# Optimization experiments

Hardware: AMD Instinct MI355X
Metric: run time of the kernel (lower is better)

The kernel has to match this reference:

```python
import math
import jax, jax.numpy as jnp
import numpy as np

# ---- static configuration (matches init_kwargs) ----
BATCH, F_IN, F_OUT = 8, 64, 128
B_IN, B_OUT = 32, 16
NL = B_OUT                    # spherical degrees l = 0..NL-1
MDIM = 2 * NL - 1             # dense order axis, m in [-(NL-1), NL-1]
N_BETA_G, N_ALPHA_G = 4, 8
MAX_BETA = math.pi / 8
N_GRID = N_BETA_G * N_ALPHA_G
SCALING = 1.0 / math.sqrt(N_GRID * F_IN * B_OUT ** 4.0 / B_IN ** 2.0)

_LF = np.concatenate([[0.0], np.cumsum(np.log(np.arange(1, 200, dtype=np.float64)))])  # log n!

def _wigner_d(l, betas):
    """Wigner small-d d^l_{m1,m2}(beta) -> [len(betas), 2l+1, 2l+1]."""
    m1 = np.arange(-l, l + 1).reshape(-1, 1, 1)
    m2 = np.arange(-l, l + 1).reshape(1, -1, 1)
    k = np.arange(0, 2 * l + 1).reshape(1, 1, -1)
    a1, a3, a4 = l + m2 - k, m1 - m2 + k, l - m1 - k
    valid = (a1 >= 0) & (a3 >= 0) & (a4 >= 0)
    logc = (0.5 * (_LF[l + m1] + _LF[l - m1] + _LF[l + m2] + _LF[l - m2])
            - _LF[np.clip(a1, 0, None)] - _LF[k]
            - _LF[np.clip(a3, 0, None)] - _LF[np.clip(a4, 0, None)])
    coef = np.where(valid, ((-1.0) ** (m1 - m2 + k)) * np.exp(logc), 0.0)
    c = np.cos(betas / 2.0)[:, None, None, None]
    s = np.sin(betas / 2.0)[:, None, None, None]
    ce = np.clip(2 * l + m2 - m1 - 2 * k, 0, None)
    se = np.clip(m1 - m2 + 2 * k, 0, None)
    return (coef[None] * (c ** ce) * (s ** se)).sum(-1)

# SOFT beta sampling grids
_betas_in = np.pi * (2 * np.arange(2 * B_IN) + 0.5) / (4 * B_IN)
_betas_out = np.pi * (2 * np.arange(2 * B_OUT) + 0.5) / (4 * B_OUT)

# Driscoll-Healy quadrature weights on the input beta grid (alpha measure 2pi/(2b) folded in)
_kk = np.arange(B_IN)
_w = ((2.0 * np.pi / (2 * B_IN)) * (2.0 / B_IN) * np.sin(_betas_in)
      * (np.sin(_betas_in[:, None] * (2 * _kk + 1)) / (2 * _kk + 1)).sum(1))

# kernel grid: s2_near_identity_grid(max_beta=pi/8, n_alpha=8, n_beta=4), beta-major order
_gb = MAX_BETA * np.arange(1, N_BETA_G + 1) / N_BETA_G
_ga = 2 * np.pi * np.arange(N_ALPHA_G) / N_ALPHA_G
GRID_BETA, GRID_ALPHA = [a.ravel() for a in np.meshgrid(_gb, _ga, indexing='ij')]

# W_ANA[beta_j, l, m]  = w_j * d^l_{m,0}(beta_j)            (S2 analysis)
# D_SYN[l, beta_k, m, n] = (2l+1) * d^l_{m,n}(beta_k)       (SO3 synthesis)
# FK[g, l, m]          = d^l_{m,0}(beta_g) * e^{i m alpha_g} (kernel real-FT, s2_rft)
W_ANA = np.zeros((2 * B_IN, NL, MDIM), np.float32)
D_SYN = np.zeros((NL, 2 * B_OUT, MDIM, MDIM), np.float32)
FK = np.zeros((N_GRID, NL, MDIM), np.complex64)
for l in range(NL):
    sl = slice(NL - 1 - l, NL + l)  # dense slots for m = -l..l
    W_ANA[:, l, sl] = (_w[:, None] * _wigner_d(l, _betas_in)[:, :, l]).astype(np.float32)
    D_SYN[l, :, sl, sl] = ((2 * l + 1) * _wigner_d(l, _betas_out)).astype(np.float32)
    m = np.arange(-l, l + 1)
    FK[:, l, sl] = (_wigner_d(l, GRID_BETA)[:, :, l]
                    * np.exp(1j * m[None, :] * GRID_ALPHA[:, None])).astype(np.complex64)
W_ANA, D_SYN, FK = jnp.asarray(W_ANA), jnp.asarray(D_SYN), jnp.asarray(FK)

_M_VALS = np.arange(-(NL - 1), NL)
_BINS_IN = _M_VALS % (2 * B_IN)  # fft bins of the alpha-frequencies m=-15..15


def setup_inputs() -> dict:
    key = jax.random.key(0)
    k1, k2 = jax.random.split(key)
    x = jax.random.normal(k1, (BATCH, F_IN, 2 * B_IN, 2 * B_IN), jnp.float32)
    kernel = jax.random.uniform(k2, (F_IN, F_OUT, N_GRID), jnp.float32, -1.0, 1.0)
    bias = jnp.zeros((1, F_OUT, 1, 1, 1), jnp.float32)
    return {"x": x, "kernel": kernel, "bias": bias}


def _s2_conv(x, kernel, bias):
    # ---- S2 FFT of the input: [B,Fin,2b_in(beta),2b_in(alpha)] -> spectrum [l,m,B,Fin] ----
    xf = jnp.fft.fft(x, axis=-1)              # e^{-i m alpha}
    xm = xf[..., _BINS_IN]                    # [B, Fin, 2b_in, MDIM]
    xhat = jnp.einsum('jlm,bfjm->lmbf', W_ANA, xm)            # [NL, MDIM, B, Fin] complex

    # ---- kernel spherical-harmonic expansion (s2_rft) ----
    kh = jnp.einsum('iog,glm->lmio', (kernel * SCALING).astype(jnp.complex64), FK)

    # ---- per-degree block matmul (s2_mm): z^l_{mn} = sum_i xhat^l_m[i] conj(kh^l_n[i]) ----
    z = jnp.einsum('lmbi,lnio->lmnbo', xhat, jnp.conj(kh))    # [NL, MDIM, MDIM, B, Fout]

    # ---- inverse SO(3) FFT: sum over degrees with (2l+1) d^l_{mn}(beta), then ifft2 over (alpha,gamma) ----
    fmn = jnp.einsum('lkmn,lmnbo->bokmn', D_SYN, z)           # [B, Fout, 2b_out, MDIM, MDIM]
    g = jnp.zeros((BATCH, F_OUT, 2 * B_OUT, 2 * B_OUT, 2 * B_OUT), fmn.dtype)
    g = g.at[..., :MDIM, :MDIM].set(fmn)
    g = jnp.roll(g, shift=(-(NL - 1), -(NL - 1)), axis=(-2, -1))  # m=0 at fft bin 0
    out = jnp.fft.ifft2(g, axes=(-2, -1)).real * float((2 * B_OUT) ** 2)  # e^{+i m alpha}
    return out.astype(jnp.float32) + bias


def reference(x, kernel, bias):
    return _s2_conv(x, kernel, bias)
```

## Files before the change

kernel.cpp:

```cpp
#include <hip/hip_runtime.h>
#include <stdint.h>
#include <math.h>


#define PI_D 3.14159265358979323846
#define SCALING_F 0.002762135864009951f

#define OFF_WANA 0
#define OFF_FKR  31744
#define OFF_FKI  47616
#define OFF_D3   63488
#define OFF_XHAT 317440
#define OFF_WT   317440
#define OFF_KHC  825344
#define OFF_Z2   3053568
#define OFF_T    11180032

typedef unsigned short u16t;
typedef __attribute__((ext_vector_type(8))) short s8v;
typedef __attribute__((ext_vector_type(8))) _Float16 h8v;
typedef __attribute__((ext_vector_type(4))) float f4v;

union frg { uint4 u; uint32_t w[4]; s8v s; h8v h; };

__device__ inline double ipow_d(double x, int e){
  double r = 1.0;
  while (e > 0){ if (e & 1) r *= x; x *= x; e >>= 1; }
  return r;
}

__device__ double wig_d(int l, int m1, int m2, double beta, const double* LF){
  double c = cos(0.5*beta), s = sin(0.5*beta);
  double sum = 0.0;
  for (int k = 0; k <= 2*l; ++k){
    int a1 = l + m2 - k, a3 = m1 - m2 + k, a4 = l - m1 - k;
    if (a1 < 0 || a3 < 0 || a4 < 0) continue;
    double logc = 0.5*(LF[l+m1]+LF[l-m1]+LF[l+m2]+LF[l-m2]) - LF[a1] - LF[k] - LF[a3] - LF[a4];
    double t = exp(logc) * ipow_d(c, a1 + a4) * ipow_d(s, a3 + k);
    sum += (a3 & 1) ? -t : t;
  }
  return sum;
}

__device__ inline uint32_t f2bf(float f){
  uint32_t u = __float_as_uint(f);
  return (u + 0x7fffu + ((u >> 16) & 1u)) >> 16;
}
__device__ inline float bf2f(uint32_t h){ return __uint_as_float((h & 0xffffu) << 16); }
__device__ inline float bf2f_lo(uint32_t h){ return __uint_as_float(h << 16); }
__device__ inline float bf2f_hi(uint32_t h){ return __uint_as_float(h & 0xffff0000u); }
__device__ inline uint32_t pack2(float a, float b){ return f2bf(a) | (f2bf(b) << 16); }

#define LF_INIT \
  __shared__ double LF[40]; \
  if (threadIdx.x == 0){ LF[0] = 0.0; double acc_ = 0.0; for (int n_ = 1; n_ < 40; ++n_){ acc_ += log((double)n_); LF[n_] = acc_; } } \
  __syncthreads();

__global__ void k_zero(float* __restrict__ ws){
  int id = blockIdx.x*256 + threadIdx.x;
  *reinterpret_cast<float4*>(ws + OFF_D3 + (size_t)id*4) = make_float4(0.f,0.f,0.f,0.f);
}

__global__ void k_consts(float* __restrict__ ws){
  LF_INIT
  int bid = blockIdx.x, tid = threadIdx.x;
  if (bid < 124){
    __shared__ double wj2[2];
    int id0 = bid*256;
    int jbase = id0/496;
    if (tid < 2){
      int j = jbase + tid;
      double wv_ = 0.0;
      if (j < 64){
        double beta = PI_D*(2*j + 0.5)/128.0;
        double wsum = 0.0;
        for (int kk = 0; kk < 32; ++kk) wsum += sin(beta*(2*kk+1))/(double)(2*kk+1);
        wv_ = (2.0*PI_D/64.0)*(2.0/32.0)*sin(beta)*wsum;
      }
      wj2[tid] = wv_;
    }
    __syncthreads();
    int id = id0 + tid;
    int m = id % 31, l = (id / 31) & 15, j = id / 496;
    int mp = m - 15, amp = mp < 0 ? -mp : mp;
    float val = 0.f;
    if (amp <= l){
      double beta = PI_D*(2*j + 0.5)/128.0;
      val = (float)(wj2[j - jbase] * wig_d(l, mp, 0, beta, LF));
    }
    ws[OFF_WANA + (l*31 + m)*64 + j] = val;
  } else if (bid < 186){
    int id = (bid - 124)*256 + tid;
    if (id >= 15872) return;
    int n = id % 31, l = (id / 31) & 15, g = id / 496;
    int np = n - 15, anp = np < 0 ? -np : np;
    float vr = 0.f, vi = 0.f;
    if (anp <= l){
      double beta = PI_D*((double)((g >> 3) + 1))/32.0;
      double alpha = (PI_D/4.0)*(double)(g & 7);
      double d = wig_d(l, np, 0, beta, LF);
      vr = (float)(d*cos(np*alpha));
      vi = (float)(d*sin(np*alpha));
    }
    ws[OFF_FKR + id] = vr;
    ws[OFF_FKI + id] = vi;
  } else if (bid < 698){
    int bb = bid - 186;
    int k = bb >> 4, l = bb & 15;
    int n21 = 2*l + 1, items = (l+1)*n21;
    double beta = PI_D*(2*k + 0.5)/64.0;
    float fl = (float)(2*l + 1);
    u16t* d3b = reinterpret_cast<u16t*>(ws + OFF_D3);
    for (int item = tid; item < items; item += 256){
      int im = item / n21, in = item - (item/n21)*n21;
      int mn = im*31 + in - l + 15;
      float v = fl * (float)wig_d(l, im, in - l, beta, LF);
      uint32_t hb = f2bf(v);
      uint32_t lb = f2bf(v - bf2f(hb));
      d3b[(mn*32 + k)*32 + l]      = (u16t)hb;
      d3b[(mn*32 + k)*32 + 16 + l] = (u16t)lb;
    }
  } else {
    u16t* wt = reinterpret_cast<u16t*>(ws + OFF_WT);
    for (int idx = tid; idx < 4096; idx += 256){
      int kidx = idx & 31, cc = (idx >> 5) & 15, h = (idx >> 9) & 1;
      int p = (idx >> 10) & 1, nt = (idx >> 11) & 1;
      int q = kidx & 1, nloc = kidx >> 1, n = h*16 + nloc, cg = nt*16 + cc;
      float val = 0.f;
      if (n <= 30){
        double th = 2.0*PI_D*(double)(((17 + n)*cg) & 31)/32.0;
        float wr = (float)cos(th), wi = (float)sin(th);
        val = p ? (q ? wr : wi) : (q ? -wi : wr);
      }
      union { _Float16 hh[2]; u16t us[2]; } cv;
      cv.hh[0] = (_Float16)val; cv.hh[1] = (_Float16)0.f;
      wt[idx] = cv.us[0];
    }
  }
}

__global__ void k_xhat(const float* __restrict__ x, float* __restrict__ ws){
  __shared__ float xl[4096];
  __shared__ float c64[64], s64[64];
  __shared__ float xmr[1024], xmi[1024];
  int tid = threadIdx.x;
  int b = blockIdx.x >> 6, i = blockIdx.x & 63;
  const float* xp = x + (b*64 + i)*4096;
  for (int idx = tid; idx < 4096; idx += 256) xl[idx] = xp[idx];
  if (tid < 64){ double a = 2.0*PI_D*tid/64.0; c64[tid] = (float)cos(a); s64[tid] = (float)sin(a); }
  __syncthreads();
  for (int item = tid; item < 1024; item += 256){
    int j = item >> 4, mi = item & 15;
    float re = 0.f, im = 0.f;
    const float* xr = xl + j*64;
    for (int a = 0; a < 64; ++a){
      int p = (mi*a) & 63;
      re += xr[a]*c64[p];
      im -= xr[a]*s64[p];
    }
    xmr[item] = re; xmi[item] = im;
  }
  __syncthreads();
  {
    int l = tid >> 4, mi = tid & 15;
    if (mi <= l){
      float rr = 0.f, ri = 0.f;
      const float* wrow = ws + OFF_WANA + (l*31 + 15 + mi)*64;
      for (int j = 0; j < 64; ++j){
        float w = wrow[j];
        rr += w * xmr[j*16 + mi];
        ri += w * xmi[j*16 + mi];
      }
      int dst = OFF_XHAT + ((l*31 + 15 + mi)*8 + b)*128 + i*2;
      ws[dst] = rr; ws[dst+1] = ri;
    }
  }
}

__global__ void k_khc(const float* __restrict__ kern, float* __restrict__ ws){
  __shared__ float kl2[32*66];
  __shared__ float fr[992], fi[992];
  int tid = threadIdx.x;
  int o = blockIdx.x >> 4, l = blockIdx.x & 15;
  for (int idx = tid; idx < 2048; idx += 256){
    int i = idx >> 5, g = idx & 31;
    kl2[g*66 + i] = kern[(i*128 + o)*32 + g];
  }
  for (int idx = tid; idx < 992; idx += 256){
    int g = idx / 31, n = idx - (idx/31)*31;
    fr[idx] = ws[OFF_FKR + g*496 + l*31 + n];
    fi[idx] = ws[OFF_FKI + g*496 + l*31 + n];
  }
  __syncthreads();
  uint32_t* khb = reinterpret_cast<uint32_t*>(ws + OFF_KHC);
  int c1 = (l*(l+1)) >> 1;
  int ntask = (l+1)*32;
  for (int t = tid; t < ntask; t += 256){
    int np = t >> 5, ip = t & 31, i0 = 2*ip;
    float ar0=0.f, ai0=0.f, ar1=0.f, ai1=0.f;
    for (int g = 0; g < 32; ++g){
      float2 kv = *reinterpret_cast<const float2*>(kl2 + g*66 + i0);
      float fv = fr[g*31 + 15 + np], gv = fi[g*31 + 15 + np];
      ar0 += kv.x*fv; ai0 -= kv.x*gv;
      ar1 += kv.y*fv; ai1 -= kv.y*gv;
    }
    size_t base = (size_t)((c1 + np)*128 + o)*64 + i0;
    khb[base]     = pack2(SCALING_F*ar0, SCALING_F*ai0);
    khb[base + 1] = pack2(SCALING_F*ar1, SCALING_F*ai1);
  }
}

__device__ inline int zswz(int o){ return (o ^ (o >> 3)) & 7; }

__global__ __launch_bounds__(512) void k_zmt(float* __restrict__ ws){
  __shared__ uint32_t lb[2][9216];
  __shared__ uint32_t zout[16384];
  int tid = threadIdx.x, lane = tid & 63, wv = tid >> 6;
  int c = lane & 15, g = lane >> 4;
  int bid = blockIdx.x;
  int b = bid / 62, t = bid - b*62;
  int nd = t >> 1, h = t & 1;
  int ndp = nd - 15, a = ndp < 0 ? -ndp : ndp;
  int neg = ndp < 0;
  int l_lo = a > 8*h ? a : 8*h;
  int l_hi = 8*h + 7;

  for (int i = tid; i < 16384; i += 512) zout[i] = 0u;

  const uint32_t* khb = reinterpret_cast<const uint32_t*>(ws + OFF_KHC);

  if (l_lo <= l_hi){
    size_t rowb = (size_t)((l_lo*(l_lo+1))/2 + a)*128;
    #pragma unroll
    for (int t4 = 0; t4 < 4; ++t4){
      int idx4 = t4*512 + tid;
      int o = idx4 >> 4, i4 = idx4 & 15;
      uint4 v = *reinterpret_cast<const uint4*>(khb + (rowb + o)*64 + i4*4);
      *reinterpret_cast<uint4*>(lb[0] + ((o*64 + i4*4) ^ ((o & 7) << 2))) = v;
    }
    int m = tid >> 5, i0 = (tid & 31)*2;
    uint32_t a0 = 0u, a1 = 0u;
    if (m <= l_lo){
      float4 xv = *reinterpret_cast<const float4*>(ws + OFF_XHAT + (((l_lo*31 + 15 + m)*8 + b)*128 + i0*2));
      a0 = pack2(xv.x, xv.y); a1 = pack2(xv.z, xv.w);
    }
    int ai_ = (m*64 + i0) ^ ((m & 7) << 2);
    lb[0][8192 + ai_] = a0; lb[0][8192 + ai_ + 1] = a1;
  }
  __syncthreads();

  int cur = 0;
  for (int l = l_lo; l <= l_hi; ++l){
    uint4 pB[4]; float4 pA = make_float4(0.f,0.f,0.f,0.f);
    int pm = tid >> 5, pi0 = (tid & 31)*2;
    bool pf = (l < l_hi);
    if (pf){
      int lx = l + 1;
      size_t rowb = (size_t)((lx*(lx+1))/2 + a)*128;
      #pragma unroll
      for (int t4 = 0; t4 < 4; ++t4){
        int idx4 = t4*512 + tid;
        int o = idx4 >> 4, i4 = idx4 & 15;
        pB[t4] = *reinterpret_cast<const uint4*>(khb + (rowb + o)*64 + i4*4);
      }
      if (pm <= lx)
        pA = *reinterpret_cast<const float4*>(ws + OFF_XHAT + (((lx*31 + 15 + pm)*8 + b)*128 + pi0*2));
    }
    uint32_t* B = lb[cur];
    uint32_t* A = lb[cur] + 8192;
    frg af[4];
    #pragma unroll
    for (int tt = 0; tt < 4; ++tt)
      af[tt].u = *reinterpret_cast<const uint4*>(A + ((c*64 + tt*16 + g*4) ^ ((c & 7) << 2)));
    int oc = wv*16 + c;
    f4v ar = {0.f,0.f,0.f,0.f}, ai = {0.f,0.f,0.f,0.f};
    #pragma unroll
    for (int tt = 0; tt < 4; ++tt){
      frg bw;
      bw.u = *reinterpret_cast<const uint4*>(B + ((oc*64 + tt*16 + g*4) ^ ((oc & 7) << 2)));
      frg br_, bi_;
      #pragma unroll
      for (int j = 0; j < 4; ++j){
        uint32_t w = bw.w[j];
        uint32_t sw = (w >> 16) | (w << 16);
        if (!neg){ br_.w[j] = w ^ 0x80000000u; bi_.w[j] = sw; }
        else if (a & 1){ br_.w[j] = w ^ 0x80008000u; bi_.w[j] = sw ^ 0x80000000u; }
        else { br_.w[j] = w; bi_.w[j] = sw ^ 0x00008000u; }
      }
      ar = __builtin_amdgcn_mfma_f32_16x16x32_bf16(af[tt].s, br_.s, ar, 0, 0, 0);
      ai = __builtin_amdgcn_mfma_f32_16x16x32_bf16(af[tt].s, bi_.s, ai, 0, 0, 0);
    }
    int lq = l - 8*h;
    #pragma unroll
    for (int rr = 0; rr < 4; ++rr){
      int m = g*4 + rr;
      zout[(m*128 + oc)*8 + (lq ^ zswz(oc))] = pack2(ar[rr], ai[rr]);
    }
    if (pf){
      uint32_t* D = lb[cur ^ 1];
      #pragma unroll
      for (int t4 = 0; t4 < 4; ++t4){
        int idx4 = t4*512 + tid;
        int o = idx4 >> 4, i4 = idx4 & 15;
        *reinterpret_cast<uint4*>(D + ((o*64 + i4*4) ^ ((o & 7) << 2))) = pB[t4];
      }
      int ai_ = (pm*64 + pi0) ^ ((pm & 7) << 2);
      uint32_t a0 = 0u, a1 = 0u;
      if (pm <= l + 1){ a0 = pack2(pA.x, pA.y); a1 = pack2(pA.z, pA.w); }
      D[8192 + ai_] = a0; D[8192 + ai_ + 1] = a1;
    }
    __syncthreads();
    cur ^= 1;
  }

  u16t* zr = reinterpret_cast<u16t*>(ws + OFF_Z2);
  u16t* zi = zr + 8126464;
  for (int idx = tid; idx < 2048; idx += 512){
    int m = idx >> 7, o = idx & 127;
    uint32_t v[8];
    #pragma unroll
    for (int lq = 0; lq < 8; ++lq) v[lq] = zout[(m*128 + o)*8 + (lq ^ zswz(o))];
    uint4 reQ = make_uint4((v[0]&0xffffu)|(v[1]<<16), (v[2]&0xffffu)|(v[3]<<16),
                           (v[4]&0xffffu)|(v[5]<<16), (v[6]&0xffffu)|(v[7]<<16));
    uint4 imQ = make_uint4((v[0]>>16)|(v[1]&0xffff0000u), (v[2]>>16)|(v[3]&0xffff0000u),
                           (v[4]>>16)|(v[5]&0xffff0000u), (v[6]>>16)|(v[7]&0xffff0000u));
    size_t base = (size_t)(m*31 + nd)*16384 + (size_t)(b*128 + o)*16 + h*8;
    *reinterpret_cast<uint4*>(zr + base) = reQ;
    *reinterpret_cast<uint4*>(zi + base) = imQ;
  }
}

__global__ __launch_bounds__(512) void k_fmt(float* __restrict__ ws){
  __shared__ uint32_t fmb[16384];
  int tid = threadIdx.x;
  int lane = tid & 63, wv = tid >> 6;
  int c = lane & 15, g = lane >> 4;
  int bt = blockIdx.x >> 4, m = blockIdx.x & 15;
  const u16t* z2r = reinterpret_cast<const u16t*>(ws + OFF_Z2);
  const u16t* z2i = z2r + 8126464;
  const u16t* d3b = reinterpret_cast<const u16t*>(ws + OFF_D3);
  const u16t* wtb = reinterpret_cast<const u16t*>(ws + OFF_WT);
  fmb[31*512 + (tid ^ 16)] = 0u;

  frg wf[2][2][2];
  #pragma unroll
  for (int nt = 0; nt < 2; ++nt)
    #pragma unroll
    for (int p = 0; p < 2; ++p)
      #pragma unroll
      for (int h = 0; h < 2; ++h)
        wf[nt][p][h].u = *reinterpret_cast<const uint4*>(wtb + ((((nt*2+p)*2+h)*16 + c)*32 + g*8));

  {
    int l0 = (g & 1)*8;
    int hl16 = (g >> 1)*16;
    size_t bo16 = (size_t)(bt*16 + c)*16;
    #pragma unroll
    for (int t = 0; t < 4; ++t){
      int nd = wv*4 + t;
      if (nd > 30) break;
      int mn = m*31 + nd;
      frg ar, ai;
      ar.u = *reinterpret_cast<const uint4*>(z2r + (size_t)mn*16384 + bo16 + l0);
      ai.u = *reinterpret_cast<const uint4*>(z2i + (size_t)mn*16384 + bo16 + l0);
      int key = ((nd >> 2) & 1) << 4;
      #pragma unroll
      for (int kh = 0; kh < 2; ++kh){
        frg bf;
        bf.u = *reinterpret_cast<const uint4*>(d3b + ((size_t)mn*32 + kh*16 + c)*32 + hl16 + l0);
        f4v z4 = {0.f, 0.f, 0.f, 0.f};
        f4v cre = __builtin_amdgcn_mfma_f32_16x16x32_bf16(ar.s, bf.s, z4, 0, 0, 0);
        f4v cim = __builtin_amdgcn_mfma_f32_16x16x32_bf16(ai.s, bf.s, z4, 0, 0, 0);
        #pragma unroll
        for (int rr = 0; rr < 4; ++rr){
          int bok = (g*4 + rr)*32 + kh*16 + c;
          union { _Float16 hh[2]; uint32_t u; } pk;
          pk.hh[0] = (_Float16)cre[rr];
          pk.hh[1] = (_Float16)cim[rr];
          fmb[nd*512 + (bok ^ key)] = pk.u;
        }
      }
    }
  }
  __syncthreads();
  uint32_t* tglob = reinterpret_cast<uint32_t*>(ws) + OFF_T;
  #pragma unroll
  for (int q = 0; q < 4; ++q){
    int mt = wv*4 + q;
    int arow = mt*16 + c;
    frg A0, A1;
    #pragma unroll
    for (int j = 0; j < 4; ++j){
      int nd0 = g*4 + j, nd1 = nd0 + 16;
      A0.w[j] = fmb[nd0*512 + (arow ^ (((nd0 >> 2) & 1) << 4))];
      A1.w[j] = fmb[nd1*512 + (arow ^ (((nd1 >> 2) & 1) << 4))];
    }
    #pragma unroll
    for (int nt = 0; nt < 2; ++nt){
      f4v z4 = {0.f, 0.f, 0.f, 0.f};
      f4v tre = __builtin_amdgcn_mfma_f32_16x16x32_f16(A0.h, wf[nt][0][0].h, z4, 0, 0, 0);
      tre     = __builtin_amdgcn_mfma_f32_16x16x32_f16(A1.h, wf[nt][0][1].h, tre, 0, 0, 0);
      f4v tim = __builtin_amdgcn_mfma_f32_16x16x32_f16(A0.h, wf[nt][1][0].h, z4, 0, 0, 0);
      tim     = __builtin_amdgcn_mfma_f32_16x16x32_f16(A1.h, wf[nt][1][1].h, tim, 0, 0, 0);
      #pragma unroll
      for (int rr = 0; rr < 4; ++rr){
        int bokl = mt*16 + g*4 + rr;
        int bokg = (bt*16 + (bokl >> 5))*32 + (bokl & 31);
        tglob[(size_t)(bokg*16 + m)*32 + nt*16 + c] = pack2(tre[rr], tim[rr]);
      }
    }
  }
}

__global__ void k_out(const float* __restrict__ bias, float* __restrict__ out,
                      const float* __restrict__ ws){
  __shared__ uint32_t tl[2048];
  __shared__ float2 tw2[32];
  int tid = threadIdx.x;
  int b4 = blockIdx.x*4;
  const uint32_t* tg = reinterpret_cast<const uint32_t*>(ws) + OFF_T + (size_t)b4*512;
  for (int idx = tid; idx < 2048; idx += 256) tl[idx] = tg[idx];
  if (tid < 32){ double a = 2.0*PI_D*tid/32.0; tw2[tid] = make_float2((float)cos(a), (float)sin(a)); }
  __syncthreads();
  int aq = tid >> 5, c = tid & 31;
  for (int q = 0; q < 4; ++q){
    int bok = b4 + q;
    const uint32_t* tq = tl + q*512;
    float t0r = bf2f(tq[c]);
    float U0=0,U1=0,U2=0,U3=0,V0=0,V1=0,V2=0,V3=0;
    int p = aq;
    #pragma unroll
    for (int m = 1; m < 16; ++m){
      uint32_t wv = tq[m*32 + c];
      float tr = bf2f_lo(wv), ti = bf2f_hi(wv);
      float2 T = tw2[p];
      float u = tr*T.x - ti*T.y;
      float v = tr*T.y + ti*T.x;
      int j = m & 3;
      if      (j == 0){ U0 += u; V0 += v; }
      else if (j == 1){ U1 += u; V1 += v; }
      else if (j == 2){ U2 += u; V2 += v; }
      else            { U3 += u; V3 += v; }
      p = (p + aq) & 31;
    }
    float bia = bias[(bok >> 5) & 127];
    float* op = out + (size_t)bok*1024 + c;
    op[aq*32]      = t0r + 2.f*(U0+U1+U2+U3) + bia;
    op[(aq+8)*32]  = t0r + 2.f*(U0-V1-U2+V3) + bia;
    op[(aq+16)*32] = t0r + 2.f*(U0-U1+U2-U3) + bia;
    op[(aq+24)*32] = t0r + 2.f*(U0+V1-U2-V3) + bia;
  }
}

extern "C" void kernel_launch(void* const* d_in, const int* in_sizes, int n_in,
                              void* d_out, int out_size, void* d_ws, size_t ws_size,
                              hipStream_t stream) {
  const float* x    = (const float*)d_in[0];
  const float* kern = (const float*)d_in[1];
  const float* bias = (const float*)d_in[2];
  float* out = (float*)d_out;
  float* ws  = (float*)d_ws;

  k_zero  <<<dim3(248),  dim3(256), 0, stream>>>(ws);
  k_consts<<<dim3(699),  dim3(256), 0, stream>>>(ws);
  k_xhat  <<<dim3(512),  dim3(256), 0, stream>>>(x, ws);
  k_khc   <<<dim3(2048), dim3(256), 0, stream>>>(kern, ws);
  k_zmt   <<<dim3(496),  dim3(512), 0, stream>>>(ws);
  k_fmt   <<<dim3(1024), dim3(512), 0, stream>>>(ws);
  k_out   <<<dim3(8192), dim3(256), 0, stream>>>(bias, out, ws);
}
```

Measured before the change: 298.2 us.

## Split k_zmt output channels across two blocks and single-buffer LDS

The per-degree complex matmul kernel now splits the 128 output channels into two halves, doubling the grid to 992 blocks of 256 threads. Double-buffered shared staging is replaced with a single buffer protected by an extra barrier, which cuts LDS use per block so more blocks fit per CU. The Z2 intermediate layout changes so each l-half is stored contiguously, and k_fmt's reads are updated to match. The aim is higher occupancy and parallelism, at the cost of an extra sync per degree and duplicated xhat loads across blocks.

```diff
diff --git a/kernel.cpp b/kernel.cpp
--- a/kernel.cpp
+++ b/kernel.cpp
@@ -212,72 +212,78 @@
 
 __device__ inline int zswz(int o){ return (o ^ (o >> 3)) & 7; }
 
-__global__ __launch_bounds__(512) void k_zmt(float* __restrict__ ws){
-  __shared__ uint32_t lb[2][9216];
-  __shared__ uint32_t zout[16384];
+__global__ __launch_bounds__(256) void k_zmt(float* __restrict__ ws){
+  __shared__ uint32_t sb[5120];
+  __shared__ uint32_t zout[8192];
   int tid = threadIdx.x, lane = tid & 63, wv = tid >> 6;
   int c = lane & 15, g = lane >> 4;
   int bid = blockIdx.x;
-  int b = bid / 62, t = bid - b*62;
-  int nd = t >> 1, h = t & 1;
+  int b  = bid / 124;
+  int r  = bid - b*124;
+  int nd = r >> 2, h = (r >> 1) & 1, oh = r & 1;
   int ndp = nd - 15, a = ndp < 0 ? -ndp : ndp;
   int neg = ndp < 0;
   int l_lo = a > 8*h ? a : 8*h;
   int l_hi = 8*h + 7;
 
-  for (int i = tid; i < 16384; i += 512) zout[i] = 0u;
+  for (int i4 = tid; i4 < 2048; i4 += 256)
+    *reinterpret_cast<uint4*>(zout + i4*4) = make_uint4(0u,0u,0u,0u);
 
   const uint32_t* khb = reinterpret_cast<const uint32_t*>(ws + OFF_KHC);
+  int pm = tid >> 4, pi = (tid & 15)*4;
 
   if (l_lo <= l_hi){
-    size_t rowb = (size_t)((l_lo*(l_lo+1))/2 + a)*128;
+    size_t rowb = ((size_t)(l_lo*(l_lo+1))/2 + a)*128 + oh*64;
     #pragma unroll
     for (int t4 = 0; t4 < 4; ++t4){
-      int idx4 = t4*512 + tid;
-      int o = idx4 >> 4, i4 = idx4 & 15;
-      uint4 v = *reinterpret_cast<const uint4*>(khb + (rowb + o)*64 + i4*4);
-      *reinterpret_cast<uint4*>(lb[0] + ((o*64 + i4*4) ^ ((o & 7) << 2))) = v;
-    }
-    int m = tid >> 5, i0 = (tid & 31)*2;
-    uint32_t a0 = 0u, a1 = 0u;
-    if (m <= l_lo){
-      float4 xv = *reinterpret_cast<const float4*>(ws + OFF_XHAT + (((l_lo*31 + 15 + m)*8 + b)*128 + i0*2));
-      a0 = pack2(xv.x, xv.y); a1 = pack2(xv.z, xv.w);
-    }
-    int ai_ = (m*64 + i0) ^ ((m & 7) << 2);
-    lb[0][8192 + ai_] = a0; lb[0][8192 + ai_ + 1] = a1;
-  }
-  __syncthreads();
-
-  int cur = 0;
+      int idx4 = t4*256 + tid;
+      int ol = idx4 >> 4, i4 = idx4 & 15;
+      uint4 v = *reinterpret_cast<const uint4*>(khb + (rowb + ol)*64 + i4*4);
+      *reinterpret_cast<uint4*>(sb + ((ol*64 + i4*4) ^ ((ol & 7) << 2))) = v;
+    }
+    uint32_t a0=0u,a1=0u,a2=0u,a3=0u;
+    if (pm <= l_lo){
+      const float* xp = ws + OFF_XHAT + (((l_lo*31 + 15 + pm)*8 + b)*128 + pi*2);
+      float4 x0 = *reinterpret_cast<const float4*>(xp);
+      float4 x1 = *reinterpret_cast<const float4*>(xp + 4);
+      a0 = pack2(x0.x,x0.y); a1 = pack2(x0.z,x0.w);
+      a2 = pack2(x1.x,x1.y); a3 = pack2(x1.z,x1.w);
+    }
+    *reinterpret_cast<uint4*>(sb + 4096 + ((pm*64 + pi) ^ ((pm & 7) << 2))) = make_uint4(a0,a1,a2,a3);
+  }
+  __syncthreads();
+
+  int ol = wv*16 + c;
   for (int l = l_lo; l <= l_hi; ++l){
-    uint4 pB[4]; float4 pA = make_float4(0.f,0.f,0.f,0.f);
-    int pm = tid >> 5, pi0 = (tid & 31)*2;
     bool pf = (l < l_hi);
+    uint4 pB[4];
+    float4 px0 = make_float4(0.f,0.f,0.f,0.f), px1 = px0;
+    bool am = false;
     if (pf){
       int lx = l + 1;
-      size_t rowb = (size_t)((lx*(lx+1))/2 + a)*128;
+      size_t rowb = ((size_t)(lx*(lx+1))/2 + a)*128 + oh*64;
       #pragma unroll
       for (int t4 = 0; t4 < 4; ++t4){
-        int idx4 = t4*512 + tid;
-        int o = idx4 >> 4, i4 = idx4 & 15;
-        pB[t4] = *reinterpret_cast<const uint4*>(khb + (rowb + o)*64 + i4*4);
-      }
-      if (pm <= lx)
-        pA = *reinterpret_cast<const float4*>(ws + OFF_XHAT + (((lx*31 + 15 + pm)*8 + b)*128 + pi0*2));
-    }
-    uint32_t* B = lb[cur];
-    uint32_t* A = lb[cur] + 8192;
+        int idx4 = t4*256 + tid;
+        int o2 = idx4 >> 4, i4 = idx4 & 15;
+        pB[t4] = *reinterpret_cast<const uint4*>(khb + (rowb + o2)*64 + i4*4);
+      }
+      am = (pm <= lx);
+      if (am){
+        const float* xp = ws + OFF_XHAT + (((lx*31 + 15 + pm)*8 + b)*128 + pi*2);
+        px0 = *reinterpret_cast<const float4*>(xp);
+        px1 = *reinterpret_cast<const float4*>(xp + 4);
+      }
+    }
     frg af[4];
     #pragma unroll
     for (int tt = 0; tt < 4; ++tt)
-      af[tt].u = *reinterpret_cast<const uint4*>(A + ((c*64 + tt*16 + g*4) ^ ((c & 7) << 2)));
-    int oc = wv*16 + c;
+      af[tt].u = *reinterpret_cast<const uint4*>(sb + 4096 + ((c*64 + tt*16 + g*4) ^ ((c & 7) << 2)));
     f4v ar = {0.f,0.f,0.f,0.f}, ai = {0.f,0.f,0.f,0.f};
     #pragma unroll
     for (int tt = 0; tt < 4; ++tt){
       frg bw;
-      bw.u = *reinterpret_cast<const uint4*>(B + ((oc*64 + tt*16 + g*4) ^ ((oc & 7) << 2)));
+      bw.u = *reinterpret_cast<const uint4*>(sb + ((ol*64 + tt*16 + g*4) ^ ((ol & 7) << 2)));
       frg br_, bi_;
       #pragma unroll
       for (int j = 0; j < 4; ++j){
@@ -294,37 +300,38 @@
     #pragma unroll
     for (int rr = 0; rr < 4; ++rr){
       int m = g*4 + rr;
-      zout[(m*128 + oc)*8 + (lq ^ zswz(oc))] = pack2(ar[rr], ai[rr]);
-    }
+      zout[(m*64 + ol)*8 + (lq ^ zswz(ol))] = pack2(ar[rr], ai[rr]);
+    }
+    __syncthreads();
     if (pf){
-      uint32_t* D = lb[cur ^ 1];
       #pragma unroll
       for (int t4 = 0; t4 < 4; ++t4){
-        int idx4 = t4*512 + tid;
-        int o = idx4 >> 4, i4 = idx4 & 15;
-        *reinterpret_cast<uint4*>(D + ((o*64 + i4*4) ^ ((o & 7) << 2))) = pB[t4];
-      }
-      int ai_ = (pm*64 + pi0) ^ ((pm & 7) << 2);
-      uint32_t a0 = 0u, a1 = 0u;
-      if (pm <= l + 1){ a0 = pack2(pA.x, pA.y); a1 = pack2(pA.z, pA.w); }
-      D[8192 + ai_] = a0; D[8192 + ai_ + 1] = a1;
+        int idx4 = t4*256 + tid;
+        int o2 = idx4 >> 4, i4 = idx4 & 15;
+        *reinterpret_cast<uint4*>(sb + ((o2*64 + i4*4) ^ ((o2 & 7) << 2))) = pB[t4];
+      }
+      uint32_t a0=0u,a1=0u,a2=0u,a3=0u;
+      if (am){
+        a0 = pack2(px0.x,px0.y); a1 = pack2(px0.z,px0.w);
+        a2 = pack2(px1.x,px1.y); a3 = pack2(px1.z,px1.w);
+      }
+      *reinterpret_cast<uint4*>(sb + 4096 + ((pm*64 + pi) ^ ((pm & 7) << 2))) = make_uint4(a0,a1,a2,a3);
     }
     __syncthreads();
-    cur ^= 1;
   }
 
   u16t* zr = reinterpret_cast<u16t*>(ws + OFF_Z2);
   u16t* zi = zr + 8126464;
-  for (int idx = tid; idx < 2048; idx += 512){
-    int m = idx >> 7, o = idx & 127;
+  for (int idx = tid; idx < 1024; idx += 256){
+    int m = idx >> 6, o = idx & 63;
     uint32_t v[8];
     #pragma unroll
-    for (int lq = 0; lq < 8; ++lq) v[lq] = zout[(m*128 + o)*8 + (lq ^ zswz(o))];
+    for (int lq = 0; lq < 8; ++lq) v[lq] = zout[(m*64 + o)*8 + (lq ^ zswz(o))];
     uint4 reQ = make_uint4((v[0]&0xffffu)|(v[1]<<16), (v[2]&0xffffu)|(v[3]<<16),
                            (v[4]&0xffffu)|(v[5]<<16), (v[6]&0xffffu)|(v[7]<<16));
     uint4 imQ = make_uint4((v[0]>>16)|(v[1]&0xffff0000u), (v[2]>>16)|(v[3]&0xffff0000u),
                            (v[4]>>16)|(v[5]&0xffff0000u), (v[6]>>16)|(v[7]&0xffff0000u));
-    size_t base = (size_t)(m*31 + nd)*16384 + (size_t)(b*128 + o)*16 + h*8;
+    size_t base = (size_t)(m*31 + nd)*16384 + (size_t)h*8192 + (size_t)(b*128 + oh*64 + o)*8;
     *reinterpret_cast<uint4*>(zr + base) = reQ;
     *reinterpret_cast<uint4*>(zi + base) = imQ;
   }
@@ -352,17 +359,17 @@
         wf[nt][p][h].u = *reinterpret_cast<const uint4*>(wtb + ((((nt*2+p)*2+h)*16 + c)*32 + g*8));
 
   {
+    int hl16 = (g >> 1)*16;
+    size_t asub = (size_t)(g & 1)*8192 + (size_t)(bt*16 + c)*8;
     int l0 = (g & 1)*8;
-    int hl16 = (g >> 1)*16;
-    size_t bo16 = (size_t)(bt*16 + c)*16;
     #pragma unroll
     for (int t = 0; t < 4; ++t){
       int nd = wv*4 + t;
       if (nd > 30) break;
       int mn = m*31 + nd;
       frg ar, ai;
-      ar.u = *reinterpret_cast<const uint4*>(z2r + (size_t)mn*16384 + bo16 + l0);
-      ai.u = *reinterpret_cast<const uint4*>(z2i + (size_t)mn*16384 + bo16 + l0);
+      ar.u = *reinterpret_cast<const uint4*>(z2r + (size_t)mn*16384 + asub);
+      ai.u = *reinterpret_cast<const uint4*>(z2i + (size_t)mn*16384 + asub);
       int key = ((nd >> 2) & 1) << 4;
       #pragma unroll
       for (int kh = 0; kh < 2; ++kh){
@@ -465,7 +472,7 @@
   k_consts<<<dim3(699),  dim3(256), 0, stream>>>(ws);
   k_xhat  <<<dim3(512),  dim3(256), 0, stream>>>(x, ws);
   k_khc   <<<dim3(2048), dim3(256), 0, stream>>>(kern, ws);
-  k_zmt   <<<dim3(496),  dim3(512), 0, stream>>>(ws);
+  k_zmt   <<<dim3(992),  dim3(256), 0, stream>>>(ws);
   k_fmt   <<<dim3(1024), dim3(512), 0, stream>>>(ws);
   k_out   <<<dim3(8192), dim3(256), 0, stream>>>(bias, out, ws);
 }
```

Result: faster. 284.9 us (-4.5%).
